# Optimization experiments

Measured on AMD Instinct MI355X. Metric: run time of the kernel, lower is better.

## Reference

```python
import jax, jax.numpy as jnp
import numpy as np

N_LINEARS = 16
CHANNELS = 3
OUTPUT_DIM = 64
Z_DIM = 128
BATCH = 512


def hash_vectors(z, n):
    # Deterministic surrogate for repo's hash_vectors: map each latent vector
    # to an integer bucket in [0, n). Data-dependent, jit-compatible.
    s = jnp.abs(jnp.sum(z, axis=1)) * 1000.0
    return jnp.mod(jnp.floor(s).astype(jnp.int32), n)


def setup_inputs() -> dict:
    key = jax.random.key(0)
    k1, k2, k3 = jax.random.split(key, 3)
    out_features = CHANNELS * OUTPUT_DIM ** 2 * N_LINEARS  # 196608
    z = jax.random.normal(k1, (BATCH, Z_DIM), dtype=jnp.float32)
    # Linear weight stored as (out_features, in_features), torch convention.
    W = jax.random.normal(k2, (out_features, Z_DIM), dtype=jnp.float32) * (1.0 / np.sqrt(Z_DIM))
    b = jax.random.normal(k3, (out_features,), dtype=jnp.float32) * 0.01
    return {"z": z, "W": W, "b": b}


def reference(z, W, b):
    B = z.shape[0]
    # Dense GEMM: (B, out_features)
    out = jnp.einsum('bi,oi->bo', z, W) + b
    out = out.reshape(B, N_LINEARS, CHANNELS, OUTPUT_DIM, OUTPUT_DIM)
    c = hash_vectors(z, N_LINEARS)  # (B,) int32 in [0, N_LINEARS)
    # Per-sample gather of one linear's output block.
    return jnp.take_along_axis(out, c[:, None, None, None, None], axis=1)[:, 0]
```

## Files before the change

kernel.cpp:

```cpp
#include <hip/hip_runtime.h>
#include <hip/hip_bf16.h>
#include <math.h>


#define N_LINEARS 16
#define ZD 128
#define BATCH 512
#define BLOCK_OUT 12288
#define SCHUNK 32
#define TJ 256

__global__ __launch_bounds__(512) void hash_kernel(
    const float* __restrict__ z, int* __restrict__ counts, int* __restrict__ lists) {
  __shared__ int cnt[N_LINEARS];
  const int tid = threadIdx.x;
  if (tid < N_LINEARS) cnt[tid] = 0;
  __syncthreads();

  const int b = tid;
  const float* zr = z + b * ZD;

  float r[8];
  #pragma unroll
  for (int j = 0; j < 8; ++j) r[j] = zr[j];
  for (int i = 8; i < ZD; i += 8) {
    #pragma unroll
    for (int j = 0; j < 8; ++j) r[j] += zr[i + j];
  }
  float res = ((r[0] + r[1]) + (r[2] + r[3])) + ((r[4] + r[5]) + (r[6] + r[7]));

  float v = fabsf(res) * 1000.0f;
  int cb = ((int)floorf(v)) & (N_LINEARS - 1);
  int pos = atomicAdd(&cnt[cb], 1);
  lists[(cb << 9) + pos] = b;

  __syncthreads();
  if (tid < N_LINEARS) counts[tid] = cnt[tid];
}

__global__ __launch_bounds__(TJ) void gen_main_kernel(
    const float* __restrict__ z, const float* __restrict__ W,
    const float* __restrict__ bias, float* __restrict__ out,
    const int* __restrict__ counts, const int* __restrict__ lists) {
  const int c = blockIdx.y;
  const int j = blockIdx.x * TJ + threadIdx.x;
  const int n = counts[c];
  if (n == 0) return;
  const int* lst = lists + (c << 9);

  const size_t row = (size_t)c * BLOCK_OUT + (size_t)j;
  const float4* __restrict__ Wv = (const float4*)(W + row * ZD);
  const float bj = bias[row];

  for (int s0 = 0; s0 < n; s0 += SCHUNK) {
    const int m = n - s0;
    float acc[SCHUNK];
    #pragma unroll
    for (int si = 0; si < SCHUNK; ++si) acc[si] = bj;

    for (int kc = 0; kc < 4; ++kc) {
      float4 w[8];
      #pragma unroll
      for (int i = 0; i < 8; ++i) w[i] = Wv[kc * 8 + i];

      #pragma unroll
      for (int si = 0; si < SCHUNK; ++si) {
        if (si < m) {
          const int bs = __builtin_amdgcn_readfirstlane(lst[s0 + si]);
          const float* __restrict__ zr = z + (size_t)bs * ZD + kc * 32;
          float a = acc[si];
          #pragma unroll
          for (int i = 0; i < 8; ++i) {
            a = fmaf(w[i].x, zr[i * 4 + 0], a);
            a = fmaf(w[i].y, zr[i * 4 + 1], a);
            a = fmaf(w[i].z, zr[i * 4 + 2], a);
            a = fmaf(w[i].w, zr[i * 4 + 3], a);
          }
          acc[si] = a;
        }
      }
    }

    #pragma unroll
    for (int si = 0; si < SCHUNK; ++si) {
      if (si < m) {
        const int bs = __builtin_amdgcn_readfirstlane(lst[s0 + si]);
        out[(size_t)bs * BLOCK_OUT + (size_t)j] = acc[si];
      }
    }
  }
}

extern "C" void kernel_launch(void* const* d_in, const int* in_sizes, int n_in,
                              void* d_out, int out_size, void* d_ws, size_t ws_size,
                              hipStream_t stream) {
  const float* z    = (const float*)d_in[0];
  const float* W    = (const float*)d_in[1];
  const float* bias = (const float*)d_in[2];
  float* out = (float*)d_out;

  int* counts = (int*)d_ws;
  int* lists  = counts + N_LINEARS;

  hipLaunchKernelGGL(hash_kernel, dim3(1), dim3(512), 0, stream, z, counts, lists);

  dim3 grid(BLOCK_OUT / TJ, N_LINEARS);
  hipLaunchKernelGGL(gen_main_kernel, grid, dim3(TJ), 0, stream,
                     z, W, bias, out, counts, lists);
}
```

Baseline: 212.0 us.

## Gather z into per-bucket transposed buffers and accumulate outer-product style

```diff
diff --git a/kernel.cpp b/kernel.cpp
--- a/kernel.cpp
+++ b/kernel.cpp
@@ -7,85 +7,100 @@
 #define ZD 128
 #define BATCH 512
 #define BLOCK_OUT 12288
-#define SCHUNK 32
+#define STILE 48
+#define SLOTS 192
 #define TJ 256
 
-__global__ __launch_bounds__(512) void hash_kernel(
-    const float* __restrict__ z, int* __restrict__ counts, int* __restrict__ lists) {
-  __shared__ int cnt[N_LINEARS];
+#define ZG_OFF_BYTES 65536
+#define ZG_FLOATS (N_LINEARS * ZD * SLOTS)
+
+__global__ __launch_bounds__(128) void hash_gather_kernel(
+    const float* __restrict__ z, int* __restrict__ counts,
+    int* __restrict__ lists, float* __restrict__ zgT) {
+  const int b = blockIdx.x;
   const int tid = threadIdx.x;
-  if (tid < N_LINEARS) cnt[tid] = 0;
-  __syncthreads();
-
-  const int b = tid;
   const float* zr = z + b * ZD;
 
-  float r[8];
-  #pragma unroll
-  for (int j = 0; j < 8; ++j) r[j] = zr[j];
-  for (int i = 8; i < ZD; i += 8) {
+  __shared__ int sh_c, sh_pos;
+
+  if (tid < 8) {
+    float r = zr[tid];
     #pragma unroll
-    for (int j = 0; j < 8; ++j) r[j] += zr[i + j];
+    for (int i = 8; i < ZD; i += 8) r += zr[i + tid];
+    float t1 = r + __shfl_down(r, 1, 64);
+    float t2 = t1 + __shfl_down(t1, 2, 64);
+    float res = t2 + __shfl_down(t2, 4, 64);
+    if (tid == 0) {
+      float v = fabsf(res) * 1000.0f;
+      int cb = ((int)floorf(v)) & (N_LINEARS - 1);
+      int pos = atomicAdd(&counts[cb], 1);
+      if (pos < SLOTS) lists[(cb << 9) + pos] = b;
+      sh_c = cb; sh_pos = pos;
+    }
   }
-  float res = ((r[0] + r[1]) + (r[2] + r[3])) + ((r[4] + r[5]) + (r[6] + r[7]));
-
-  float v = fabsf(res) * 1000.0f;
-  int cb = ((int)floorf(v)) & (N_LINEARS - 1);
-  int pos = atomicAdd(&cnt[cb], 1);
-  lists[(cb << 9) + pos] = b;
-
   __syncthreads();
-  if (tid < N_LINEARS) counts[tid] = cnt[tid];
+  const int c = sh_c, pos = sh_pos;
+  if (pos < SLOTS) {
+    zgT[(size_t)c * (ZD * SLOTS) + (size_t)tid * SLOTS + pos] = zr[tid];
+  }
 }
 
 __global__ __launch_bounds__(TJ) void gen_main_kernel(
-    const float* __restrict__ z, const float* __restrict__ W,
-    const float* __restrict__ bias, float* __restrict__ out,
-    const int* __restrict__ counts, const int* __restrict__ lists) {
+    const float* __restrict__ W, const float* __restrict__ bias,
+    float* __restrict__ out, const int* __restrict__ counts,
+    const int* __restrict__ lists, const float* __restrict__ zgT) {
   const int c = blockIdx.y;
   const int j = blockIdx.x * TJ + threadIdx.x;
-  const int n = counts[c];
+  const int n0 = counts[c];
+  const int n = n0 > SLOTS ? SLOTS : n0;
   if (n == 0) return;
-  const int* lst = lists + (c << 9);
 
   const size_t row = (size_t)c * BLOCK_OUT + (size_t)j;
-  const float4* __restrict__ Wv = (const float4*)(W + row * ZD);
+  const float4* __restrict__ Wv = (const float4*)(W + row * (size_t)ZD);
   const float bj = bias[row];
+  const float* __restrict__ zt = zgT + (size_t)c * (ZD * SLOTS);
+  const int* __restrict__ lst = lists + (c << 9);
 
-  for (int s0 = 0; s0 < n; s0 += SCHUNK) {
-    const int m = n - s0;
-    float acc[SCHUNK];
+  for (int s0 = 0; s0 < n; s0 += STILE) {
+    float acc[STILE];
     #pragma unroll
-    for (int si = 0; si < SCHUNK; ++si) acc[si] = bj;
+    for (int t = 0; t < STILE; ++t) acc[t] = bj;
 
-    for (int kc = 0; kc < 4; ++kc) {
-      float4 w[8];
+    float4 zb[2][STILE / 4];
+    {
+      const float4* zr0 = (const float4*)(zt + s0);
       #pragma unroll
-      for (int i = 0; i < 8; ++i) w[i] = Wv[kc * 8 + i];
+      for (int t = 0; t < STILE / 4; ++t) zb[0][t] = zr0[t];
+    }
 
+    float4 wq = Wv[0];
+    #pragma unroll 4
+    for (int k = 0; k < ZD; ++k) {
+      const int cur = k & 1;
+      if (k + 1 < ZD) {
+        const float4* zrn = (const float4*)(zt + (size_t)(k + 1) * SLOTS + s0);
+        #pragma unroll
+        for (int t = 0; t < STILE / 4; ++t) zb[cur ^ 1][t] = zrn[t];
+      }
+      const int kr = k & 3;
+      const float wk = kr == 0 ? wq.x : kr == 1 ? wq.y : kr == 2 ? wq.z : wq.w;
+      if (kr == 3 && k + 1 < ZD) wq = Wv[(k + 1) >> 2];
       #pragma unroll
-      for (int si = 0; si < SCHUNK; ++si) {
-        if (si < m) {
-          const int bs = __builtin_amdgcn_readfirstlane(lst[s0 + si]);
-          const float* __restrict__ zr = z + (size_t)bs * ZD + kc * 32;
-          float a = acc[si];
-          #pragma unroll
-          for (int i = 0; i < 8; ++i) {
-            a = fmaf(w[i].x, zr[i * 4 + 0], a);
-            a = fmaf(w[i].y, zr[i * 4 + 1], a);
-            a = fmaf(w[i].z, zr[i * 4 + 2], a);
-            a = fmaf(w[i].w, zr[i * 4 + 3], a);
-          }
-          acc[si] = a;
-        }
+      for (int t = 0; t < STILE / 4; ++t) {
+        const float4 zv = zb[cur][t];
+        acc[4 * t + 0] = fmaf(wk, zv.x, acc[4 * t + 0]);
+        acc[4 * t + 1] = fmaf(wk, zv.y, acc[4 * t + 1]);
+        acc[4 * t + 2] = fmaf(wk, zv.z, acc[4 * t + 2]);
+        acc[4 * t + 3] = fmaf(wk, zv.w, acc[4 * t + 3]);
       }
     }
 
+    const int m = n - s0;
     #pragma unroll
-    for (int si = 0; si < SCHUNK; ++si) {
-      if (si < m) {
-        const int bs = __builtin_amdgcn_readfirstlane(lst[s0 + si]);
-        out[(size_t)bs * BLOCK_OUT + (size_t)j] = acc[si];
+    for (int t = 0; t < STILE; ++t) {
+      if (t < m) {
+        const int bs = lst[s0 + t];
+        out[(size_t)bs * BLOCK_OUT + (size_t)j] = acc[t];
       }
     }
   }
@@ -100,11 +115,15 @@
   float* out = (float*)d_out;
 
   int* counts = (int*)d_ws;
-  int* lists  = counts + N_LINEARS;
+  int* lists  = counts + 16;
+  float* zgT  = (float*)((char*)d_ws + ZG_OFF_BYTES);
 
-  hipLaunchKernelGGL(hash_kernel, dim3(1), dim3(512), 0, stream, z, counts, lists);
+  hipMemsetAsync(d_ws, 0, ZG_OFF_BYTES + ZG_FLOATS * sizeof(float), stream);
+
+  hipLaunchKernelGGL(hash_gather_kernel, dim3(BATCH), dim3(128), 0, stream,
+                     z, counts, lists, zgT);
 
   dim3 grid(BLOCK_OUT / TJ, N_LINEARS);
   hipLaunchKernelGGL(gen_main_kernel, grid, dim3(TJ), 0, stream,
-                     z, W, bias, out, counts, lists);
+                     W, bias, out, counts, lists, zgT);
 }
```

Result: slower. 267.5 us (+26.2%).
